# Performance work log

Hardware: AMD Instinct MI355X
Metric: run time of the kernel (lower is better)

Reference implementation:

```python
import jax, jax.numpy as jnp
import numpy as np

D_MODEL = 1024
N_STATE = 16
D_INNER = 2 * D_MODEL          # 2048
DT_RANK = (D_MODEL + 15) // 16  # 64 = ceil(d/16)
K_CONV = 4
B, L = 1, 1024


def setup_inputs() -> dict:
    key = jax.random.key(0)
    ks = jax.random.split(key, 9)
    s = lambda fan_in: 1.0 / np.sqrt(fan_in)
    x = jax.random.normal(ks[0], (B, L, D_MODEL), dtype=jnp.float32)
    W_in = jax.random.normal(ks[1], (D_MODEL, 2 * D_INNER), dtype=jnp.float32) * s(D_MODEL)
    conv_w = jax.random.normal(ks[2], (D_INNER, K_CONV), dtype=jnp.float32) * s(K_CONV)
    conv_b = jnp.zeros((D_INNER,), dtype=jnp.float32)
    W_x = jax.random.normal(ks[3], (D_INNER, DT_RANK + 2 * N_STATE), dtype=jnp.float32) * s(D_INNER)
    W_dt = jax.random.normal(ks[4], (DT_RANK, D_INNER), dtype=jnp.float32) * s(DT_RANK)
    b_dt = jax.random.normal(ks[5], (D_INNER,), dtype=jnp.float32) * 0.01
    # A_log initialized as log(1..N) repeated over d_inner, as in __init__
    A_log = jnp.log(jnp.broadcast_to(jnp.arange(1, N_STATE + 1, dtype=jnp.float32), (D_INNER, N_STATE)))
    D = jnp.ones((D_INNER,), dtype=jnp.float32)
    W_out = jax.random.normal(ks[6], (D_INNER, D_MODEL), dtype=jnp.float32) * s(D_INNER)
    return {"x": x, "W_in": W_in, "conv_w": conv_w, "conv_b": conv_b,
            "W_x": W_x, "W_dt": W_dt, "b_dt": b_dt, "A_log": A_log,
            "D": D, "W_out": W_out}


def _causal_dw_conv(x, w, b):
    # x: [B,L,C], w: [C,K], b: [C]; causal depthwise conv (pad left K-1)
    K = w.shape[1]
    xp = jnp.pad(x, ((0, 0), (K - 1, 0), (0, 0)))
    Lx = x.shape[1]
    out = b
    for k in range(K):  # small fixed K=4
        out = out + xp[:, k:k + Lx, :] * w[:, k]
    return out


def _selective_scan(u, delta, A, Bm, Cm, D):
    # u,delta: [B,L,Di]; A: [Di,N]; Bm,Cm: [B,L,N]; D: [Di]
    dA = jnp.exp(delta[..., None] * A)                      # [B,L,Di,N]
    dBu = delta[..., None] * Bm[:, :, None, :] * u[..., None]
    dA_t = jnp.moveaxis(dA, 1, 0)    # [L,B,Di,N]
    dBu_t = jnp.moveaxis(dBu, 1, 0)
    C_t = jnp.moveaxis(Cm, 1, 0)     # [L,B,N]

    def step(h, inp):
        dA_i, dBu_i, C_i = inp
        h = dA_i * h + dBu_i
        y = jnp.einsum('bdn,bn->bd', h, C_i)
        return h, y

    h0 = jnp.zeros(u.shape[:1] + A.shape, dtype=u.dtype)  # [B,Di,N]
    _, ys = jax.lax.scan(step, h0, (dA_t, dBu_t, C_t))
    y = jnp.moveaxis(ys, 0, 1)       # [B,L,Di]
    return y + u * D


def reference(x, W_in, conv_w, conv_b, W_x, W_dt, b_dt, A_log, D, W_out):
    silu = jax.nn.silu
    x_and_res = x @ W_in                                   # [B,L,2*Di]
    x_in, res = jnp.split(x_and_res, 2, axis=-1)
    x_conv = silu(_causal_dw_conv(x_in, conv_w, conv_b))   # [B,L,Di]
    x_dbl = x_conv @ W_x                                   # [B,L,dt_rank+2N]
    dt, Bm, Cm = jnp.split(x_dbl, [DT_RANK, DT_RANK + N_STATE], axis=-1)
    delta = jax.nn.softplus(dt @ W_dt + b_dt)              # [B,L,Di]
    A = -jnp.exp(A_log)                                    # [Di,N]
    y = _selective_scan(x_conv, delta, A, Bm, Cm, D)
    return (y * silu(res)) @ W_out                         # [B,L,d_model]
```

## Files before the change

### kernel.cpp

```cpp
#include <hip/hip_runtime.h>

typedef unsigned short u16;
typedef unsigned int u32;
typedef __attribute__((ext_vector_type(8))) short bf16x8;
typedef __attribute__((ext_vector_type(4))) float f32x4;

#define LSEQ 1024
#define NSL 8

__device__ __forceinline__ float b2f(u16 v) { return __uint_as_float(((u32)v) << 16); }
__device__ __forceinline__ u16 f2b(float f) {
    u32 x = __float_as_uint(f);
    return (u16)((x + 0x7fffu + ((x >> 16) & 1u)) >> 16);
}
__device__ __forceinline__ float rdf(const void* p, size_t i, int f) {
    return f ? b2f(((const u16*)p)[i]) : ((const float*)p)[i];
}
__device__ __forceinline__ float fsig(float x) {
    return __builtin_amdgcn_rcpf(1.f + __expf(-x));
}

typedef const __attribute__((address_space(1))) u32* gp_t;
typedef __attribute__((address_space(3))) u32* lp_t;
__device__ __forceinline__ void gload16(const u16* g, u16* lds_wave_base) {
    __builtin_amdgcn_global_load_lds((gp_t)g, (lp_t)lds_wave_base, 16, 0, 0);
}

__global__ __launch_bounds__(256) void prep_k(const void* __restrict__ x,
                                              const void* __restrict__ W_in,
                                              const void* __restrict__ W_out,
                                              const void* __restrict__ W_x,
                                              const void* __restrict__ W_dt,
                                              u16* __restrict__ xb,
                                              u16* __restrict__ W_in_t,
                                              u16* __restrict__ W_out_t,
                                              u16* __restrict__ W_x_t,
                                              u16* __restrict__ W_dt_t,
                                              int* __restrict__ flag) {
    __shared__ int cnt;
    __shared__ __align__(8) u16 tile[32][36];
    if (threadIdx.x == 0) cnt = 0;
    __syncthreads();
    const u16* xu = (const u16*)x;
    int c = 0;
#pragma unroll
    for (int j = 0; j < 8; ++j) {
        u16 u = xu[threadIdx.x * 8 + j];
        int e = (u >> 7) & 0xFF;
        c += (e == 0 || (e >= 100 && e <= 140)) ? 1 : 0;
    }
    atomicAdd(&cnt, c);
    __syncthreads();
    const int f = (cnt >= 1638) ? 1 : 0;
    if (blockIdx.x == 0 && threadIdx.x == 0) *flag = f;

    int blk = blockIdx.x;
    if (blk < 1024) {
        int i = (blk * 256 + threadIdx.x) * 4;
        ushort4 o;
        if (f) {
            o = *(const ushort4*)(xu + i);
        } else {
            float4 v = *(const float4*)((const float*)x + i);
            o = make_ushort4(f2b(v.x), f2b(v.y), f2b(v.z), f2b(v.w));
        }
        *(ushort4*)(xb + i) = o;
        return;
    }
    blk -= 1024;
    const void* src; u16* dst; int R, Cn, nbc, t;
    if (blk < 4096)      { src = W_in;  dst = W_in_t;  R = 1024; Cn = 4096; nbc = 128; t = blk; }
    else if (blk < 6144) { src = W_out; dst = W_out_t; R = 2048; Cn = 1024; nbc = 32;  t = blk - 4096; }
    else if (blk < 6400) { src = W_x;   dst = W_x_t;   R = 2048; Cn = 96;   nbc = 4;   t = blk - 6144; }
    else                 { src = W_dt;  dst = W_dt_t;  R = 64;   Cn = 2048; nbc = 64;  t = blk - 6400; }
    int br = t / nbc, bc = t - br * nbc;
    int r0 = br * 32, c0 = bc * 32;
    {
        int ty = threadIdx.x >> 3, tx4 = (threadIdx.x & 7) << 2;
        u16 o0 = 0, o1 = 0, o2 = 0, o3 = 0;
        if (c0 + tx4 < Cn) {
            size_t off = (size_t)(r0 + ty) * Cn + c0 + tx4;
            if (f) {
                ushort4 u = *(const ushort4*)((const u16*)src + off);
                o0 = u.x; o1 = u.y; o2 = u.z; o3 = u.w;
            } else {
                float4 v = *(const float4*)((const float*)src + off);
                o0 = f2b(v.x); o1 = f2b(v.y); o2 = f2b(v.z); o3 = f2b(v.w);
            }
        }
        *(ushort4*)(&tile[ty][tx4]) = make_ushort4(o0, o1, o2, o3);
    }
    __syncthreads();
    {
        int cc = threadIdx.x >> 3, r4 = (threadIdx.x & 7) << 2;
        ushort4 o = make_ushort4(tile[r4][cc], tile[r4 + 1][cc], tile[r4 + 2][cc], tile[r4 + 3][cc]);
        *(ushort4*)(dst + (size_t)(c0 + cc) * R + r0 + r4) = o;
    }
}

template <int MT, int NT, int OUT_MODE>
__global__ __launch_bounds__(256) void gemm_bt(const u16* __restrict__ A,
                                               const u16* __restrict__ Bt,
                                               void* __restrict__ C,
                                               int M, int N, int K,
                                               const int* __restrict__ flag) {
    constexpr int BM = 32 * MT, BN = 32 * NT;
    __shared__ __align__(16) u16 As[2][2 * BM * 32];
    __shared__ __align__(16) u16 Bs[2][2 * BN * 32];
    const int tid = threadIdx.x;
    const int w = tid >> 6, lane = tid & 63;
    const int wm = w & 1, wn = w >> 1;
    const int m_blk = blockIdx.x * BM, n_blk = blockIdx.y * BN;
    const int lm = lane & 15, lq = lane >> 4;
    const int sr = lane >> 2, sc = (lane & 3) << 3;
    const int f = (OUT_MODE == 2) ? flag[0] : 0;

    f32x4 acc[MT][NT];
#pragma unroll
    for (int i = 0; i < MT; ++i)
#pragma unroll
        for (int j = 0; j < NT; ++j) acc[i][j] = (f32x4){0.f, 0.f, 0.f, 0.f};

    auto stage = [&](int buf, int kb) {
#pragma unroll
        for (int cch = 0; cch < 2; ++cch) {
#pragma unroll
            for (int i = 0; i < BM / 64; ++i) {
                int row = i * 64 + w * 16;
                gload16(A + (size_t)(m_blk + row + sr) * K + kb + cch * 32 + sc,
                        &As[buf][cch * BM * 32 + row * 32]);
            }
#pragma unroll
            for (int i = 0; i < BN / 64; ++i) {
                int row = i * 64 + w * 16;
                gload16(Bt + (size_t)(n_blk + row + sr) * K + kb + cch * 32 + sc,
                        &Bs[buf][cch * BN * 32 + row * 32]);
            }
        }
    };
    auto compute = [&](int buf) {
#pragma unroll
        for (int cch = 0; cch < 2; ++cch) {
            bf16x8 af[MT], bf[NT];
#pragma unroll
            for (int tm = 0; tm < MT; ++tm)
                af[tm] = *(const bf16x8*)(&As[buf][cch * BM * 32 +
                                                   (wm * 16 * MT + tm * 16 + lm) * 32 + lq * 8]);
#pragma unroll
            for (int tn = 0; tn < NT; ++tn)
                bf[tn] = *(const bf16x8*)(&Bs[buf][cch * BN * 32 +
                                                   (wn * 16 * NT + tn * 16 + lm) * 32 + lq * 8]);
#pragma unroll
            for (int tm = 0; tm < MT; ++tm)
#pragma unroll
                for (int tn = 0; tn < NT; ++tn)
                    acc[tm][tn] = __builtin_amdgcn_mfma_f32_16x16x32_bf16(af[tm], bf[tn],
                                                                          acc[tm][tn], 0, 0, 0);
        }
    };

    stage(0, 0);
    __syncthreads();
    int cur = 0;
    for (int kb = 64; kb < K; kb += 64) {
        stage(cur ^ 1, kb);
        compute(cur);
        __syncthreads();
        cur ^= 1;
    }
    compute(cur);

#pragma unroll
    for (int tm = 0; tm < MT; ++tm)
#pragma unroll
        for (int tn = 0; tn < NT; ++tn)
#pragma unroll
            for (int r = 0; r < 4; ++r) {
                int row = m_blk + wm * 16 * MT + tm * 16 + lq * 4 + r;
                int col = n_blk + wn * 16 * NT + tn * 16 + lm;
                float v = acc[tm][tn][r];
                if (OUT_MODE == 1) {
                    ((u16*)C)[(size_t)row * N + col] = f2b(v);
                } else {
                    if (f) ((u16*)C)[(size_t)row * N + col] = f2b(v);
                    else   ((float*)C)[(size_t)row * N + col] = v;
                }
            }
}

__global__ __launch_bounds__(256) void gemm2_conv_k(const u16* __restrict__ xz,
                                                    const u16* __restrict__ Bt,
                                                    float* __restrict__ parts,
                                                    u16* __restrict__ xconv,
                                                    const void* __restrict__ cw,
                                                    const void* __restrict__ cb,
                                                    const int* __restrict__ flag) {
    constexpr int MT = 2, NT = 4;
    constexpr int BM = 64, BN = 128, K = 2048, KLEN = 256;
    __shared__ __align__(16) u16 As[2][2 * BM * 32];
    __shared__ __align__(16) u16 Bs[2][2 * BN * 32];
    __shared__ __align__(16) float cws[KLEN * 4];
    __shared__ float cbs[KLEN];
    const int tid = threadIdx.x;
    const int w = tid >> 6, lane = tid & 63;
    const int wm = w & 1, wn = w >> 1;
    const int m_blk = blockIdx.x * BM;
    const int kb0 = blockIdx.z * KLEN;
    const int lm = lane & 15, lq = lane >> 4;
    const int sr = lane >> 2, sc = (lane & 3) << 3;
    const int f = flag[0];

    {
#pragma unroll
        for (int k = 0; k < 4; ++k) cws[tid * 4 + k] = rdf(cw, (size_t)(kb0 + tid) * 4 + k, f);
        cbs[tid] = rdf(cb, kb0 + tid, f);
    }
    __syncthreads();

    f32x4 acc[MT][NT];
#pragma unroll
    for (int i = 0; i < MT; ++i)
#pragma unroll
        for (int j = 0; j < NT; ++j) acc[i][j] = (f32x4){0.f, 0.f, 0.f, 0.f};

    const int arow = tid >> 2;
    const int acg = (tid & 3) << 3;
    const int trow = m_blk + arow;

    auto bstage = [&](int buf, int kb) {
#pragma unroll
        for (int cch = 0; cch < 2; ++cch)
#pragma unroll
            for (int i = 0; i < BN / 64; ++i) {
                int row = i * 64 + w * 16;
                gload16(Bt + (size_t)(row + sr) * K + kb + cch * 32 + sc,
                        &Bs[buf][cch * BN * 32 + row * 32]);
            }
    };
    auto astage = [&](int buf, int cch, int kbase) {
        const int d = kbase + acg;
        const int dl = kbase - kb0 + acg;
        bf16x8 xv[4];
#pragma unroll
        for (int kk = 0; kk < 4; ++kk) {
            bf16x8 zz = {0, 0, 0, 0, 0, 0, 0, 0};
            int tt = trow + kk - 3;
            xv[kk] = (tt >= 0) ? *(const bf16x8*)(xz + (size_t)tt * 4096 + d) : zz;
        }
        bf16x8 rv;
#pragma unroll
        for (int j = 0; j < 8; ++j) {
            f32x4 wv = *(const f32x4*)(cws + (dl + j) * 4);
            float a = cbs[dl + j];
#pragma unroll
            for (int kk = 0; kk < 4; ++kk) a += b2f((u16)xv[kk][j]) * wv[kk];
            rv[j] = (short)f2b(a * fsig(a));
        }
        *(bf16x8*)(&As[buf][cch * BM * 32 + arow * 32 + acg]) = rv;
        *(bf16x8*)(xconv + (size_t)trow * 2048 + d) = rv;
    };
    auto compute = [&](int buf) {
#pragma unroll
        for (int cch = 0; cch < 2; ++cch) {
            bf16x8 af[MT], bf[NT];
#pragma unroll
            for (int tm = 0; tm < MT; ++tm)
                af[tm] = *(const bf16x8*)(&As[buf][cch * BM * 32 +
                                                   (wm * 32 + tm * 16 + lm) * 32 + lq * 8]);
#pragma unroll
            for (int tn = 0; tn < NT; ++tn)
                bf[tn] = *(const bf16x8*)(&Bs[buf][cch * BN * 32 +
                                                   (wn * 64 + tn * 16 + lm) * 32 + lq * 8]);
#pragma unroll
            for (int tm = 0; tm < MT; ++tm)
#pragma unroll
                for (int tn = 0; tn < NT; ++tn)
                    acc[tm][tn] = __builtin_amdgcn_mfma_f32_16x16x32_bf16(af[tm], bf[tn],
                                                                          acc[tm][tn], 0, 0, 0);
        }
    };

    bstage(0, kb0);
    astage(0, 0, kb0);
    astage(0, 1, kb0 + 32);
    __syncthreads();
    int cur = 0;
    for (int kb = kb0 + 64; kb < kb0 + KLEN; kb += 64) {
        bstage(cur ^ 1, kb);
        astage(cur ^ 1, 0, kb);
        astage(cur ^ 1, 1, kb + 32);
        compute(cur);
        __syncthreads();
        cur ^= 1;
    }
    compute(cur);

#pragma unroll
    for (int tm = 0; tm < MT; ++tm)
#pragma unroll
        for (int tn = 0; tn < NT; ++tn)
#pragma unroll
            for (int r = 0; r < 4; ++r) {
                int row = m_blk + wm * 32 + tm * 16 + lq * 4 + r;
                int col = wn * 64 + tn * 16 + lm;
                parts[(size_t)blockIdx.z * 131072 + (size_t)row * 128 + col] = acc[tm][tn][r];
            }
}

__device__ __forceinline__ void delta_tile(const float* __restrict__ parts,
                                           const u16* __restrict__ Wdt,
                                           const void* __restrict__ bias,
                                           int f, int t0, int d0,
                                           u16* As2, u16* Bs2, float (*dlt)[128],
                                           int tid, int w, int lm, int lq, int sr, int sc) {
#pragma unroll
    for (int cch = 0; cch < 2; ++cch)
#pragma unroll
        for (int i = 0; i < 2; ++i) {
            int row = i * 64 + w * 16;
            gload16(Wdt + (size_t)(d0 + row + sr) * 64 + cch * 32 + sc,
                    Bs2 + cch * 4096 + row * 32);
        }
    {
        int arow = tid >> 3, acg = (tid & 7) << 3;
        f32x4 s0 = {0.f, 0.f, 0.f, 0.f}, s1 = {0.f, 0.f, 0.f, 0.f};
#pragma unroll
        for (int sl = 0; sl < NSL; ++sl) {
            const float* p = parts + (size_t)sl * 131072 + (size_t)(t0 + arow) * 128 + acg;
            s0 += *(const f32x4*)p;
            s1 += *(const f32x4*)(p + 4);
        }
        bf16x8 rv;
#pragma unroll
        for (int j = 0; j < 4; ++j) {
            rv[j] = (short)f2b(s0[j]);
            rv[4 + j] = (short)f2b(s1[j]);
        }
        *(bf16x8*)(As2 + (acg >> 5) * 1024 + arow * 32 + (acg & 31)) = rv;
    }
    __syncthreads();

    f32x4 dacc[2][2];
#pragma unroll
    for (int i = 0; i < 2; ++i)
#pragma unroll
        for (int j = 0; j < 2; ++j) dacc[i][j] = (f32x4){0.f, 0.f, 0.f, 0.f};
#pragma unroll
    for (int cch = 0; cch < 2; ++cch) {
        bf16x8 af[2], bf[2];
#pragma unroll
        for (int tm = 0; tm < 2; ++tm)
            af[tm] = *(const bf16x8*)(As2 + cch * 1024 + (tm * 16 + lm) * 32 + lq * 8);
#pragma unroll
        for (int tn = 0; tn < 2; ++tn)
            bf[tn] = *(const bf16x8*)(Bs2 + cch * 4096 + (w * 32 + tn * 16 + lm) * 32 + lq * 8);
#pragma unroll
        for (int tm = 0; tm < 2; ++tm)
#pragma unroll
            for (int tn = 0; tn < 2; ++tn)
                dacc[tm][tn] = __builtin_amdgcn_mfma_f32_16x16x32_bf16(af[tm], bf[tn],
                                                                       dacc[tm][tn], 0, 0, 0);
    }
#pragma unroll
    for (int tm = 0; tm < 2; ++tm)
#pragma unroll
        for (int tn = 0; tn < 2; ++tn)
#pragma unroll
            for (int r = 0; r < 4; ++r) {
                int row = tm * 16 + lq * 4 + r;
                int col = w * 32 + tn * 16 + lm;
                float b = rdf(bias, d0 + col, f);
                float t2 = dacc[tm][tn][r] + b;
                dlt[row][col] = fmaxf(t2, 0.f) + __logf(1.f + __expf(-fabsf(t2)));
            }
    __syncthreads();
}

__global__ __launch_bounds__(256) void scan1_k(const u16* __restrict__ xc,
                                               const float* __restrict__ parts,
                                               const u16* __restrict__ Wdt,
                                               const void* __restrict__ bias,
                                               const void* __restrict__ A_log,
                                               float* __restrict__ Acar,
                                               float* __restrict__ Bcar,
                                               float* __restrict__ deltag,
                                               float* __restrict__ bcg,
                                               const int* __restrict__ flag) {
    __shared__ __align__(16) u16 As2[2 * 32 * 32];
    __shared__ __align__(16) u16 Bs2[2 * 128 * 32];
    __shared__ __align__(16) float dlt[32][128];
    __shared__ __align__(16) float BCs[32][32];
    const int f = *flag;
    const int tid = threadIdx.x, b = blockIdx.x;
    const int w = tid >> 6, lane = tid & 63;
    const int lm = lane & 15, lq = lane >> 4;
    const int sr = lane >> 2, sc = (lane & 3) << 3;
    const int c = b >> 4, dblk = b & 15;
    const int d0 = dblk * 128;
    const int t0 = c * 32;
    {
        int idx = tid * 4;
        int tl = idx >> 5, col = idx & 31;
        f32x4 s = {0.f, 0.f, 0.f, 0.f};
#pragma unroll
        for (int sl = 0; sl < NSL; ++sl)
            s += *(const f32x4*)(parts + (size_t)sl * 131072 + (size_t)(t0 + tl) * 128 + 64 + col);
        *(f32x4*)&BCs[tl][col] = s;
    }
    delta_tile(parts, Wdt, bias, f, t0, d0, As2, Bs2, dlt, tid, w, lm, lq, sr, sc);

#pragma unroll
    for (int k = 0; k < 4; ++k) {
        int kk = tid + k * 256;
        int row = kk >> 5, col4 = (kk & 31) << 2;
        *(f32x4*)(deltag + (size_t)(t0 + row) * 2048 + d0 + col4) = *(const f32x4*)&dlt[row][col4];
    }
    if (dblk == 0) {
        int idx = tid * 4;
        int tl = idx >> 5, col = idx & 31;
        *(f32x4*)(bcg + c * 1024 + tl * 32 + col) = *(const f32x4*)&BCs[tl][col];
    }

    const int dl = tid >> 1, nh = tid & 1;
    const int d = d0 + dl, n0 = nh << 3;
    float A[8], P[8], h[8];
#pragma unroll
    for (int j = 0; j < 8; ++j) {
        A[j] = -__expf(rdf(A_log, d * 16 + n0 + j, f));
        P[j] = 1.f;
        h[j] = 0.f;
    }
#pragma unroll 4
    for (int i = 0; i < 32; ++i) {
        int t = t0 + i;
        float de = dlt[i][dl];
        float dBu = de * b2f(xc[t * 2048 + d]);
        f32x4 Bv0 = *(const f32x4*)&BCs[i][n0];
        f32x4 Bv1 = *(const f32x4*)&BCs[i][n0 + 4];
#pragma unroll
        for (int j = 0; j < 8; ++j) {
            float Bv = (j < 4) ? Bv0[j & 3] : Bv1[j & 3];
            float a = __expf(de * A[j]);
            h[j] = a * h[j] + Bv * dBu;
            P[j] *= a;
        }
    }
    f32x4 pa0 = {P[0], P[1], P[2], P[3]}, pa1 = {P[4], P[5], P[6], P[7]};
    f32x4 hb0 = {h[0], h[1], h[2], h[3]}, hb1 = {h[4], h[5], h[6], h[7]};
    size_t base = (size_t)c * 32768 + d * 16 + n0;
    *(f32x4*)(Acar + base) = pa0;
    *(f32x4*)(Acar + base + 4) = pa1;
    *(f32x4*)(Bcar + base) = hb0;
    *(f32x4*)(Bcar + base + 4) = hb1;
}

__global__ __launch_bounds__(256) void scan3_k(const u16* __restrict__ xc,
                                               const float* __restrict__ deltag,
                                               const float* __restrict__ bcg,
                                               const u16* __restrict__ xz,
                                               const void* __restrict__ A_log,
                                               const void* __restrict__ Dvp,
                                               const float* __restrict__ Acar,
                                               const float* __restrict__ Bcar,
                                               u16* __restrict__ yg,
                                               const int* __restrict__ flag) {
    __shared__ __align__(16) float dlt[32][128];
    __shared__ __align__(16) float BCs[32][32];
    const int f = *flag;
    const int tid = threadIdx.x, b = blockIdx.x;
    const int c = b >> 4;
    const int d0 = (b & 15) * 128;
    const int t0 = c * 32;
    {
        int idx = tid * 4;
        int tl = idx >> 5, col = idx & 31;
        *(f32x4*)&BCs[tl][col] = *(const f32x4*)(bcg + c * 1024 + tl * 32 + col);
    }
#pragma unroll
    for (int k = 0; k < 4; ++k) {
        int kk = tid + k * 256;
        int row = kk >> 5, col4 = (kk & 31) << 2;
        *(f32x4*)&dlt[row][col4] = *(const f32x4*)(deltag + (size_t)(t0 + row) * 2048 + d0 + col4);
    }
    __syncthreads();

    const int dl = tid >> 1, nh = tid & 1;
    const int d = d0 + dl, n0 = nh << 3;
    float A[8], h[8];
#pragma unroll
    for (int j = 0; j < 8; ++j) {
        A[j] = -__expf(rdf(A_log, d * 16 + n0 + j, f));
        h[j] = 0.f;
    }
    for (int cc = 0; cc < c; ++cc) {
        size_t cb = (size_t)cc * 32768 + d * 16 + n0;
        f32x4 a0 = *(const f32x4*)(Acar + cb);
        f32x4 a1 = *(const f32x4*)(Acar + cb + 4);
        f32x4 b0 = *(const f32x4*)(Bcar + cb);
        f32x4 b1 = *(const f32x4*)(Bcar + cb + 4);
#pragma unroll
        for (int j = 0; j < 4; ++j) {
            h[j] = a0[j] * h[j] + b0[j];
            h[4 + j] = a1[j] * h[4 + j] + b1[j];
        }
    }

    float Dd = rdf(Dvp, d, f);
#pragma unroll 4
    for (int i = 0; i < 32; ++i) {
        int t = t0 + i;
        float de = dlt[i][dl];
        float u = b2f(xc[t * 2048 + d]);
        float dBu = de * u;
        f32x4 Bv0 = *(const f32x4*)&BCs[i][n0];
        f32x4 Bv1 = *(const f32x4*)&BCs[i][n0 + 4];
        f32x4 Cv0 = *(const f32x4*)&BCs[i][16 + n0];
        f32x4 Cv1 = *(const f32x4*)&BCs[i][20 + n0];
        float p = 0.f;
#pragma unroll
        for (int j = 0; j < 8; ++j) {
            float Bv = (j < 4) ? Bv0[j & 3] : Bv1[j & 3];
            float Cv = (j < 4) ? Cv0[j & 3] : Cv1[j & 3];
            float a = __expf(de * A[j]);
            h[j] = a * h[j] + Bv * dBu;
            p += h[j] * Cv;
        }
        p += __shfl_xor(p, 1);
        if (nh == 0) {
            float r = b2f(xz[(size_t)t * 4096 + 2048 + d]);
            float yt = p + u * Dd;
            yg[t * 2048 + d] = f2b(yt * r * fsig(r));
        }
    }
}

__global__ __launch_bounds__(256) void gemm3_red_k(const float* __restrict__ parts,
                                                   const u16* __restrict__ Bt,
                                                   float* __restrict__ delta,
                                                   const void* __restrict__ bias,
                                                   const int* __restrict__ flag) {
    constexpr int MT = 2, NT = 2, BM = 64, BN = 64, K = 64;
    __shared__ __align__(16) u16 As[2 * BM * 32];
    __shared__ __align__(16) u16 Bs[2 * BN * 32];
    const int tid = threadIdx.x;
    const int w = tid >> 6, lane = tid & 63;
    const int wm = w & 1, wn = w >> 1;
    const int m_blk = blockIdx.x * BM, n_blk = blockIdx.y * BN;
    const int lm = lane & 15, lq = lane >> 4;
    const int sr = lane >> 2, sc = (lane & 3) << 3;
    const int f = flag[0];

    f32x4 acc[MT][NT];
#pragma unroll
    for (int i = 0; i < MT; ++i)
#pragma unroll
        for (int j = 0; j < NT; ++j) acc[i][j] = (f32x4){0.f, 0.f, 0.f, 0.f};

    const int arow = tid >> 2;
    const int acg = (tid & 3) << 3;

#pragma unroll
    for (int cch = 0; cch < 2; ++cch) {
        int row = w * 16;
        gload16(Bt + (size_t)(n_blk + row + sr) * K + cch * 32 + sc, &Bs[cch * BN * 32 + row * 32]);
    }
#pragma unroll
    for (int cch = 0; cch < 2; ++cch) {
        f32x4 s0 = {0.f, 0.f, 0.f, 0.f}, s1 = {0.f, 0.f, 0.f, 0.f};
#pragma unroll
        for (int sl = 0; sl < NSL; ++sl) {
            const float* p = parts + (size_t)sl * 131072 + (size_t)(m_blk + arow) * 128 + cch * 32 + acg;
            s0 += *(const f32x4*)p;
            s1 += *(const f32x4*)(p + 4);
        }
        bf16x8 rv;
#pragma unroll
        for (int j = 0; j < 4; ++j) {
            rv[j] = (short)f2b(s0[j]);
            rv[4 + j] = (short)f2b(s1[j]);
        }
        *(bf16x8*)(&As[cch * BM * 32 + arow * 32 + acg]) = rv;
    }
    __syncthreads();

#pragma unroll
    for (int cch = 0; cch < 2; ++cch) {
        bf16x8 af[MT], bf[NT];
#pragma unroll
        for (int tm = 0; tm < MT; ++tm)
            af[tm] = *(const bf16x8*)(&As[cch * BM * 32 + (wm * 32 + tm * 16 + lm) * 32 + lq * 8]);
#pragma unroll
        for (int tn = 0; tn < NT; ++tn)
            bf[tn] = *(const bf16x8*)(&Bs[cch * BN * 32 + (wn * 32 + tn * 16 + lm) * 32 + lq * 8]);
#pragma unroll
        for (int tm = 0; tm < MT; ++tm)
#pragma unroll
            for (int tn = 0; tn < NT; ++tn)
                acc[tm][tn] = __builtin_amdgcn_mfma_f32_16x16x32_bf16(af[tm], bf[tn],
                                                                      acc[tm][tn], 0, 0, 0);
    }

#pragma unroll
    for (int tm = 0; tm < MT; ++tm)
#pragma unroll
        for (int tn = 0; tn < NT; ++tn)
#pragma unroll
            for (int r = 0; r < 4; ++r) {
                int row = m_blk + wm * 32 + tm * 16 + lq * 4 + r;
                int col = n_blk + wn * 32 + tn * 16 + lm;
                float b = rdf(bias, col, f);
                float t2 = acc[tm][tn][r] + b;
                float sp = fmaxf(t2, 0.f) + __logf(1.f + __expf(-fabsf(t2)));
                delta[(size_t)row * 2048 + col] = sp;
            }
}

__global__ __launch_bounds__(256) void scan_k(const float* __restrict__ delta,
                                              const u16* __restrict__ xc,
                                              const float* __restrict__ parts,
                                              const u16* __restrict__ xz,
                                              const void* __restrict__ A_log,
                                              const void* __restrict__ Dvp,
                                              u16* __restrict__ yg,
                                              const int* __restrict__ flag) {
    int f = *flag;
    int g = blockIdx.x * 256 + threadIdx.x;
    int d = g >> 4, n = g & 15;
    float A = -__expf(rdf(A_log, d * 16 + n, f));
    float Dd = rdf(Dvp, d, f);
    float h = 0.f;
    for (int t = 0; t < LSEQ; ++t) {
        float de = delta[t * 2048 + d];
        float u = b2f(xc[t * 2048 + d]);
        float Bv = 0.f, Cv = 0.f;
#pragma unroll
        for (int sl = 0; sl < NSL; ++sl) {
            Bv += parts[(size_t)sl * 131072 + (size_t)t * 128 + 64 + n];
            Cv += parts[(size_t)sl * 131072 + (size_t)t * 128 + 80 + n];
        }
        h = __expf(de * A) * h + (de * Bv) * u;
        float p = h * Cv;
        p += __shfl_xor(p, 1);
        p += __shfl_xor(p, 2);
        p += __shfl_xor(p, 4);
        p += __shfl_xor(p, 8);
        if (n == 0) {
            float r = b2f(xz[(size_t)t * 4096 + 2048 + d]);
            float yt = p + u * Dd;
            yg[t * 2048 + d] = f2b(yt * r * fsig(r));
        }
    }
}

extern "C" void kernel_launch(void* const* d_in, const int* in_sizes, int n_in,
                              void* d_out, int out_size, void* d_ws, size_t ws_size,
                              hipStream_t stream) {
    const void* x      = d_in[0];
    const void* W_in   = d_in[1];
    const void* conv_w = d_in[2];
    const void* conv_b = d_in[3];
    const void* W_x    = d_in[4];
    const void* W_dt   = d_in[5];
    const void* b_dt   = d_in[6];
    const void* A_log  = d_in[7];
    const void* Dv     = d_in[8];
    const void* W_out  = d_in[9];

    char* ws = (char*)d_ws;
    u16*   xz     = (u16*)(ws);
    u16*   xconv  = (u16*)(ws + 8388608);
    float* parts  = (float*)(ws + 12582912);
    u16*   W_in_t = (u16*)(ws + 16777216);
    u16*   yg     = (u16*)(ws + 25165824);
    u16*   xb     = (u16*)(ws + 25165824);
    u16*   W_x_t  = (u16*)(ws + 29360128);
    u16*   W_dt_t = (u16*)(ws + 29884416);
    u16*   W_out_t= (u16*)(ws + 30146560);
    int*   flag   = (int*)(ws + 34340864);
    float* Acar   = (float*)(ws + 34340992);
    float* Bcar   = (float*)(ws + 38535296);
    float* deltag = (float*)(ws + 42729600);
    float* bcg    = (float*)(ws + 51118208);
    float* dfb    = (float*)(ws + 34340992);
    const bool chunked_ok = (ws_size >= 51249280);

    prep_k<<<7552, 256, 0, stream>>>(x, W_in, W_out, W_x, W_dt,
                                     xb, W_in_t, W_out_t, W_x_t, W_dt_t, flag);
    gemm_bt<2, 4, 1><<<dim3(16, 32), 256, 0, stream>>>(xb, W_in_t, (void*)xz,
                                                       1024, 4096, 1024, flag);
    gemm2_conv_k<<<dim3(16, 1, 8), 256, 0, stream>>>(xz, W_x_t, parts, xconv,
                                                     conv_w, conv_b, flag);

    if (chunked_ok) {
        scan1_k<<<512, 256, 0, stream>>>(xconv, parts, W_dt_t, b_dt, A_log, Acar, Bcar,
                                         deltag, bcg, flag);
        scan3_k<<<512, 256, 0, stream>>>(xconv, deltag, bcg, xz, A_log, Dv,
                                         Acar, Bcar, yg, flag);
    } else {
        gemm3_red_k<<<dim3(16, 32), 256, 0, stream>>>(parts, W_dt_t, dfb, b_dt, flag);
        scan_k<<<128, 256, 0, stream>>>(dfb, xconv, parts, xz, A_log, Dv, yg, flag);
    }

    gemm_bt<2, 2, 2><<<dim3(16, 16), 256, 0, stream>>>(yg, W_out_t, d_out,
                                                       1024, 1024, 2048, flag);
}
```

Before: 205.3 us.

## Overlap non-critical weight transposes with the input-projection GEMM launch

```diff
diff --git a/kernel.cpp b/kernel.cpp
--- a/kernel.cpp
+++ b/kernel.cpp
@@ -26,54 +26,8 @@
     __builtin_amdgcn_global_load_lds((gp_t)g, (lp_t)lds_wave_base, 16, 0, 0);
 }
 
-__global__ __launch_bounds__(256) void prep_k(const void* __restrict__ x,
-                                              const void* __restrict__ W_in,
-                                              const void* __restrict__ W_out,
-                                              const void* __restrict__ W_x,
-                                              const void* __restrict__ W_dt,
-                                              u16* __restrict__ xb,
-                                              u16* __restrict__ W_in_t,
-                                              u16* __restrict__ W_out_t,
-                                              u16* __restrict__ W_x_t,
-                                              u16* __restrict__ W_dt_t,
-                                              int* __restrict__ flag) {
-    __shared__ int cnt;
-    __shared__ __align__(8) u16 tile[32][36];
-    if (threadIdx.x == 0) cnt = 0;
-    __syncthreads();
-    const u16* xu = (const u16*)x;
-    int c = 0;
-#pragma unroll
-    for (int j = 0; j < 8; ++j) {
-        u16 u = xu[threadIdx.x * 8 + j];
-        int e = (u >> 7) & 0xFF;
-        c += (e == 0 || (e >= 100 && e <= 140)) ? 1 : 0;
-    }
-    atomicAdd(&cnt, c);
-    __syncthreads();
-    const int f = (cnt >= 1638) ? 1 : 0;
-    if (blockIdx.x == 0 && threadIdx.x == 0) *flag = f;
-
-    int blk = blockIdx.x;
-    if (blk < 1024) {
-        int i = (blk * 256 + threadIdx.x) * 4;
-        ushort4 o;
-        if (f) {
-            o = *(const ushort4*)(xu + i);
-        } else {
-            float4 v = *(const float4*)((const float*)x + i);
-            o = make_ushort4(f2b(v.x), f2b(v.y), f2b(v.z), f2b(v.w));
-        }
-        *(ushort4*)(xb + i) = o;
-        return;
-    }
-    blk -= 1024;
-    const void* src; u16* dst; int R, Cn, nbc, t;
-    if (blk < 4096)      { src = W_in;  dst = W_in_t;  R = 1024; Cn = 4096; nbc = 128; t = blk; }
-    else if (blk < 6144) { src = W_out; dst = W_out_t; R = 2048; Cn = 1024; nbc = 32;  t = blk - 4096; }
-    else if (blk < 6400) { src = W_x;   dst = W_x_t;   R = 2048; Cn = 96;   nbc = 4;   t = blk - 6144; }
-    else                 { src = W_dt;  dst = W_dt_t;  R = 64;   Cn = 2048; nbc = 64;  t = blk - 6400; }
-    int br = t / nbc, bc = t - br * nbc;
+__device__ __forceinline__ void transpose_tile(const void* src, u16* dst, int R, int Cn,
+                                               int br, int bc, int f, u16 (*tile)[36]) {
     int r0 = br * 32, c0 = bc * 32;
     {
         int ty = threadIdx.x >> 3, tx4 = (threadIdx.x & 7) << 2;
@@ -96,6 +50,143 @@
         ushort4 o = make_ushort4(tile[r4][cc], tile[r4 + 1][cc], tile[r4 + 2][cc], tile[r4 + 3][cc]);
         *(ushort4*)(dst + (size_t)(c0 + cc) * R + r0 + r4) = o;
     }
+}
+
+__global__ __launch_bounds__(256) void prep_k(const void* __restrict__ x,
+                                              const void* __restrict__ W_in,
+                                              u16* __restrict__ xb,
+                                              u16* __restrict__ W_in_t,
+                                              int* __restrict__ flag) {
+    __shared__ int cnt;
+    __shared__ __align__(8) u16 tile[32][36];
+    if (threadIdx.x == 0) cnt = 0;
+    __syncthreads();
+    const u16* xu = (const u16*)x;
+    int c = 0;
+#pragma unroll
+    for (int j = 0; j < 8; ++j) {
+        u16 u = xu[threadIdx.x * 8 + j];
+        int e = (u >> 7) & 0xFF;
+        c += (e == 0 || (e >= 100 && e <= 140)) ? 1 : 0;
+    }
+    atomicAdd(&cnt, c);
+    __syncthreads();
+    const int f = (cnt >= 1638) ? 1 : 0;
+    if (blockIdx.x == 0 && threadIdx.x == 0) *flag = f;
+
+    int blk = blockIdx.x;
+    if (blk < 1024) {
+        int i = (blk * 256 + threadIdx.x) * 4;
+        ushort4 o;
+        if (f) {
+            o = *(const ushort4*)(xu + i);
+        } else {
+            float4 v = *(const float4*)((const float*)x + i);
+            o = make_ushort4(f2b(v.x), f2b(v.y), f2b(v.z), f2b(v.w));
+        }
+        *(ushort4*)(xb + i) = o;
+        return;
+    }
+    blk -= 1024;
+    transpose_tile(W_in, W_in_t, 1024, 4096, blk / 128, blk % 128, f, tile);
+}
+
+__global__ __launch_bounds__(256) void gemm1_fat_k(const u16* __restrict__ A,
+                                                   const u16* __restrict__ Bt,
+                                                   u16* __restrict__ C,
+                                                   const void* __restrict__ W_out,
+                                                   const void* __restrict__ W_x,
+                                                   const void* __restrict__ W_dt,
+                                                   u16* __restrict__ W_out_t,
+                                                   u16* __restrict__ W_x_t,
+                                                   u16* __restrict__ W_dt_t,
+                                                   const int* __restrict__ flag) {
+    constexpr int MT = 2, NT = 4, BM = 64, BN = 128, N = 4096, K = 1024;
+    __shared__ __align__(16) u16 As[2][2 * BM * 32];
+    __shared__ __align__(16) u16 Bs[2][2 * BN * 32];
+    __shared__ __align__(8) u16 tile[32][36];
+    if (blockIdx.y >= 32) {
+        int id = (blockIdx.y - 32) * 16 + blockIdx.x;
+        const int f = flag[0];
+        const void* src; u16* dst; int R, Cn, nbc, t;
+        if (id < 2048)      { src = W_out; dst = W_out_t; R = 2048; Cn = 1024; nbc = 32; t = id; }
+        else if (id < 2304) { src = W_x;   dst = W_x_t;   R = 2048; Cn = 96;   nbc = 4;  t = id - 2048; }
+        else                { src = W_dt;  dst = W_dt_t;  R = 64;   Cn = 2048; nbc = 64; t = id - 2304; }
+        transpose_tile(src, dst, R, Cn, t / nbc, t % nbc, f, tile);
+        return;
+    }
+    const int tid = threadIdx.x;
+    const int w = tid >> 6, lane = tid & 63;
+    const int wm = w & 1, wn = w >> 1;
+    const int m_blk = blockIdx.x * BM, n_blk = blockIdx.y * BN;
+    const int lm = lane & 15, lq = lane >> 4;
+    const int sr = lane >> 2, sc = (lane & 3) << 3;
+
+    f32x4 acc[MT][NT];
+#pragma unroll
+    for (int i = 0; i < MT; ++i)
+#pragma unroll
+        for (int j = 0; j < NT; ++j) acc[i][j] = (f32x4){0.f, 0.f, 0.f, 0.f};
+
+    auto stage = [&](int buf, int kb) {
+#pragma unroll
+        for (int cch = 0; cch < 2; ++cch) {
+#pragma unroll
+            for (int i = 0; i < BM / 64; ++i) {
+                int row = i * 64 + w * 16;
+                gload16(A + (size_t)(m_blk + row + sr) * K + kb + cch * 32 + sc,
+                        &As[buf][cch * BM * 32 + row * 32]);
+            }
+#pragma unroll
+            for (int i = 0; i < BN / 64; ++i) {
+                int row = i * 64 + w * 16;
+                gload16(Bt + (size_t)(n_blk + row + sr) * K + kb + cch * 32 + sc,
+                        &Bs[buf][cch * BN * 32 + row * 32]);
+            }
+        }
+    };
+    auto compute = [&](int buf) {
+#pragma unroll
+        for (int cch = 0; cch < 2; ++cch) {
+            bf16x8 af[MT], bf[NT];
+#pragma unroll
+            for (int tm = 0; tm < MT; ++tm)
+                af[tm] = *(const bf16x8*)(&As[buf][cch * BM * 32 +
+                                                   (wm * 16 * MT + tm * 16 + lm) * 32 + lq * 8]);
+#pragma unroll
+            for (int tn = 0; tn < NT; ++tn)
+                bf[tn] = *(const bf16x8*)(&Bs[buf][cch * BN * 32 +
+                                                   (wn * 16 * NT + tn * 16 + lm) * 32 + lq * 8]);
+#pragma unroll
+            for (int tm = 0; tm < MT; ++tm)
+#pragma unroll
+                for (int tn = 0; tn < NT; ++tn)
+                    acc[tm][tn] = __builtin_amdgcn_mfma_f32_16x16x32_bf16(af[tm], bf[tn],
+                                                                          acc[tm][tn], 0, 0, 0);
+        }
+    };
+
+    stage(0, 0);
+    __syncthreads();
+    int cur = 0;
+    for (int kb = 64; kb < K; kb += 64) {
+        stage(cur ^ 1, kb);
+        compute(cur);
+        __syncthreads();
+        cur ^= 1;
+    }
+    compute(cur);
+
+#pragma unroll
+    for (int tm = 0; tm < MT; ++tm)
+#pragma unroll
+        for (int tn = 0; tn < NT; ++tn)
+#pragma unroll
+            for (int r = 0; r < 4; ++r) {
+                int row = m_blk + wm * 16 * MT + tm * 16 + lq * 4 + r;
+                int col = n_blk + wn * 16 * NT + tn * 16 + lm;
+                C[(size_t)row * N + col] = f2b(acc[tm][tn][r]);
+            }
 }
 
 template <int MT, int NT, int OUT_MODE>
@@ -587,10 +678,10 @@
     for (int cch = 0; cch < 2; ++cch) {
         bf16x8 af[MT], bf[NT];
 #pragma unroll
-        for (int tm = 0; tm < MT; ++tm)
+        for (int tm = 0; tm < 2; ++tm)
             af[tm] = *(const bf16x8*)(&As[cch * BM * 32 + (wm * 32 + tm * 16 + lm) * 32 + lq * 8]);
 #pragma unroll
-        for (int tn = 0; tn < NT; ++tn)
+        for (int tn = 0; tn < 2; ++tn)
             bf[tn] = *(const bf16x8*)(&Bs[cch * BN * 32 + (wn * 32 + tn * 16 + lm) * 32 + lq * 8]);
 #pragma unroll
         for (int tm = 0; tm < MT; ++tm)
@@ -684,10 +775,10 @@
     float* dfb    = (float*)(ws + 34340992);
     const bool chunked_ok = (ws_size >= 51249280);
 
-    prep_k<<<7552, 256, 0, stream>>>(x, W_in, W_out, W_x, W_dt,
-                                     xb, W_in_t, W_out_t, W_x_t, W_dt_t, flag);
-    gemm_bt<2, 4, 1><<<dim3(16, 32), 256, 0, stream>>>(xb, W_in_t, (void*)xz,
-                                                       1024, 4096, 1024, flag);
+    prep_k<<<5120, 256, 0, stream>>>(x, W_in, xb, W_in_t, flag);
+    gemm1_fat_k<<<dim3(16, 184), 256, 0, stream>>>(xb, W_in_t, xz,
+                                                   W_out, W_x, W_dt,
+                                                   W_out_t, W_x_t, W_dt_t, flag);
     gemm2_conv_k<<<dim3(16, 1, 8), 256, 0, stream>>>(xz, W_x_t, parts, xconv,
                                                      conv_w, conv_b, flag);
 
```

Measured after the change: 202.1 us. Within noise of the previous version (-1.6%).
